# Kernel optimization log

Measured on AMD Instinct MI355X. Metric: run time of the kernel, lower is better.

Reference implementation:

```python
import jax, jax.numpy as jnp
import numpy as np

B, S, H = 2, 2048, 1024
N, DK = 16, 64          # heads, key/value dim (N*DK == H)
DF = 4096               # FFN hidden
SCALE = 1.0 / float(DK) ** 0.5
EPS = 1e-5


def _layer_norm(x, g, b):
    mu = jnp.mean(x, axis=-1, keepdims=True)
    var = jnp.var(x, axis=-1, keepdims=True)
    return (x - mu) * jax.lax.rsqrt(var + EPS) * g + b


def setup_inputs() -> dict:
    key = jax.random.key(0)
    ks = jax.random.split(key, 12)
    s = 0.02
    return {
        "x": jax.random.normal(ks[0], (B, S, H), dtype=jnp.float32),
        "Wq": jax.random.normal(ks[1], (N * DK, H), dtype=jnp.float32) * s,
        "bq": jnp.zeros((N * DK,), jnp.float32),
        "Wk": jax.random.normal(ks[2], (N * DK, H), dtype=jnp.float32) * s,
        "bk": jnp.zeros((N * DK,), jnp.float32),
        "Wv": jax.random.normal(ks[3], (N * DK, H), dtype=jnp.float32) * s,
        "bv": jnp.zeros((N * DK,), jnp.float32),
        "Wo": jax.random.normal(ks[4], (H, N * DK), dtype=jnp.float32) * s,
        "bo": jnp.zeros((H,), jnp.float32),
        "W1": jax.random.normal(ks[5], (DF, H), dtype=jnp.float32) * s,
        "b1": jnp.zeros((DF,), jnp.float32),
        "W2": jax.random.normal(ks[6], (H, DF), dtype=jnp.float32) * s,
        "b2": jnp.zeros((H,), jnp.float32),
        "ln1_g": jnp.ones((H,), jnp.float32),
        "ln1_b": jnp.zeros((H,), jnp.float32),
        "ln2_g": jnp.ones((H,), jnp.float32),
        "ln2_b": jnp.zeros((H,), jnp.float32),
    }


def _mha(x, Wq, bq, Wk, bk, Wv, bv, Wo, bo):
    b = x.shape[0]
    q = (x @ Wq.T + bq).reshape(b, -1, N, DK)  # [B,T,N,DK]
    k = (x @ Wk.T + bk).reshape(b, -1, N, DK)
    v = (x @ Wv.T + bv).reshape(b, -1, N, DK)
    # naive full-score attention, faithful to torch einsum layout
    scores = jnp.einsum('btnd,bsnd->tsbn', q, k) * SCALE  # [T,S,B,N]
    p = jax.nn.softmax(scores, axis=1)                    # softmax over S (dim=1)
    attn = jnp.einsum('tsbn,bsnd->btnd', p, v)            # [B,T,N,DK]
    attn = attn.reshape(b, attn.shape[1], -1)             # [B,T,N*DK]
    return attn @ Wo.T + bo


def reference(x, Wq, bq, Wk, bk, Wv, bv, Wo, bo, W1, b1, W2, b2,
              ln1_g, ln1_b, ln2_g, ln2_b):
    # post-LN encoder layer: x = LN(x + MHA(x)); x = LN(x + FFN(x))
    h = _layer_norm(x + _mha(x, Wq, bq, Wk, bk, Wv, bv, Wo, bo), ln1_g, ln1_b)
    ff = jax.nn.relu(h @ W1.T + b1) @ W2.T + b2
    return _layer_norm(h + ff, ln2_g, ln2_b)
```

## Files before the change

kernel.cpp:

```cpp
#include <hip/hip_runtime.h>
#include <stdint.h>


typedef unsigned short u16;
typedef __bf16 bf16x8 __attribute__((ext_vector_type(8)));
typedef float  f32x4  __attribute__((ext_vector_type(4)));

__device__ __forceinline__ u16 f2bf(float f) {
    unsigned int u = __float_as_uint(f);
    u += 0x7FFFu + ((u >> 16) & 1u);
    return (u16)(u >> 16);
}

__device__ __forceinline__ float bf2f(u16 v) {
    return __uint_as_float((unsigned)v << 16);
}

__device__ __forceinline__ unsigned pack_bf16_hi(float lo, float hi) {
#if __has_builtin(__builtin_amdgcn_perm)
    return __builtin_amdgcn_perm(__float_as_uint(hi), __float_as_uint(lo), 0x07060302u);
#else
    return (__float_as_uint(lo) >> 16) | (__float_as_uint(hi) & 0xFFFF0000u);
#endif
}

__device__ __forceinline__ void async_load16(const u16* g, u16* l) {
    __builtin_amdgcn_global_load_lds(
        (__attribute__((address_space(1))) void*)g,
        (__attribute__((address_space(3))) void*)l, 16, 0, 0);
}

struct CvtArgs {
    const float* src[7];
    u16*         dst[7];
    int          n[7];
};

__global__ __launch_bounds__(256) void k_cvt_all(CvtArgs a) {
    const int seg = blockIdx.y;
    const int i = (blockIdx.x * 256 + threadIdx.x) * 8;
    if (i >= a.n[seg]) return;
    const float* in = a.src[seg];
    u16* out = a.dst[seg];
    float4 x = *(const float4*)(in + i);
    float4 y = *(const float4*)(in + i + 4);
    uint4 o;
    o.x = (unsigned)f2bf(x.x) | ((unsigned)f2bf(x.y) << 16);
    o.y = (unsigned)f2bf(x.z) | ((unsigned)f2bf(x.w) << 16);
    o.z = (unsigned)f2bf(y.x) | ((unsigned)f2bf(y.y) << 16);
    o.w = (unsigned)f2bf(y.z) | ((unsigned)f2bf(y.w) << 16);
    *(uint4*)(out + i) = o;
}

__global__ __launch_bounds__(256) void k_concat3(const float* __restrict__ a,
                                                 const float* __restrict__ b,
                                                 const float* __restrict__ c,
                                                 float* __restrict__ out) {
    int i = blockIdx.x * 256 + threadIdx.x;
    if (i >= 3072) return;
    out[i] = (i < 1024) ? a[i] : (i < 2048 ? b[i - 1024] : c[i - 2048]);
}

template<int OUT_BF16, int RELU>
__global__ __launch_bounds__(256, 4) void k_gemm_bt(
    const u16* __restrict__ A, const u16* __restrict__ Bw,
    const float* __restrict__ bias, void* __restrict__ Y,
    int M, int N, int K)
{
    __shared__ u16 As[128 * 64];
    __shared__ u16 Bs[128 * 64];
    const int tid  = threadIdx.x;
    const int wave = tid >> 6, lane = tid & 63;
    const int lm = lane & 15, lq = lane >> 4;
    const int m0 = blockIdx.x * 128, n0 = blockIdx.y * 128;
    const int wr = (wave >> 1) * 64, wc = (wave & 1) * 64;

    const int ksz = K / gridDim.z;
    const int ks  = blockIdx.z * ksz, ke = ks + ksz;

    const int sr8 = wave * 8 + (lane >> 3);
    const int scx = ((lane & 7) * 8) ^ (((sr8 >> 2) & 3) << 4);
    const size_t arow = (size_t)(m0 + sr8) * K + scx;
    const size_t brow = (size_t)(n0 + sr8) * K + scx;
    const int sw = ((lm >> 2) & 3) << 4;

    f32x4 acc[4][4];
#pragma unroll
    for (int i = 0; i < 4; i++)
#pragma unroll
        for (int j = 0; j < 4; j++) acc[i][j] = (f32x4){0.f, 0.f, 0.f, 0.f};

    for (int k0 = ks; k0 < ke; k0 += 64) {
        __syncthreads();
#pragma unroll
        for (int j = 0; j < 4; j++) {
            async_load16(A  + arow + (size_t)(j * 32) * K + k0, As + j * 2048 + wave * 512);
            async_load16(Bw + brow + (size_t)(j * 32) * K + k0, Bs + j * 2048 + wave * 512);
        }
        __syncthreads();

#pragma unroll
        for (int h = 0; h < 2; h++) {
            const int cofs = (h * 32 + lq * 8) ^ sw;
            bf16x8 af[4], bf[4];
#pragma unroll
            for (int i = 0; i < 4; i++)
                af[i] = *(const bf16x8*)(As + (wr + i * 16 + lm) * 64 + cofs);
#pragma unroll
            for (int j = 0; j < 4; j++)
                bf[j] = *(const bf16x8*)(Bs + (wc + j * 16 + lm) * 64 + cofs);
#pragma unroll
            for (int i = 0; i < 4; i++)
#pragma unroll
                for (int j = 0; j < 4; j++)
                    acc[i][j] = __builtin_amdgcn_mfma_f32_16x16x32_bf16(af[i], bf[j], acc[i][j], 0, 0, 0);
        }
    }

    const float bsc = (blockIdx.z == 0) ? 1.f : 0.f;
    const size_t zoff = (size_t)blockIdx.z * M * N;
#pragma unroll
    for (int i = 0; i < 4; i++) {
        const int mg = m0 + wr + i * 16 + lq * 4;
#pragma unroll
        for (int j = 0; j < 4; j++) {
            const int ng = n0 + wc + j * 16 + lm;
            const float bv = bias[ng] * bsc;
#pragma unroll
            for (int r = 0; r < 4; r++) {
                float v = acc[i][j][r] + bv;
                if (RELU) v = fmaxf(v, 0.f);
                if (OUT_BF16) ((u16*)Y)[zoff + (size_t)(mg + r) * N + ng] = f2bf(v);
                else          ((float*)Y)[zoff + (size_t)(mg + r) * N + ng] = v;
            }
        }
    }
}

__global__ __launch_bounds__(256) void k_transpose_v(const u16* __restrict__ qkv,
                                                     u16* __restrict__ vt) {
    __shared__ u16 T[64 * 72];
    const int tid = threadIdx.x;
    const int t0 = blockIdx.x * 64;
    const int bn = blockIdx.y;
    const int b = bn >> 4, n = bn & 15;
    {
        const int r = tid >> 2, c = (tid & 3) * 16;
        const u16* src = qkv + (size_t)(b * 2048 + t0 + r) * 3072 + 2048 + n * 64 + c;
        *(uint4*)&T[r * 72 + c]     = *(const uint4*)(src);
        *(uint4*)&T[r * 72 + c + 8] = *(const uint4*)(src + 8);
    }
    __syncthreads();
    {
        const int d = tid >> 2, c = (tid & 3) * 16;
        union { u16 h[16]; uint4 v[2]; } tmp;
#pragma unroll
        for (int j = 0; j < 16; j++) {
            const int w = c + j;
            const int k = ((w & 3) << 4) + (w >> 2);
            tmp.h[j] = T[k * 72 + d];
        }
        u16* dst = vt + (size_t)(bn * 64 + d) * 2048 + t0 + c;
        *(uint4*)(dst)     = tmp.v[0];
        *(uint4*)(dst + 8) = tmp.v[1];
    }
}

__global__ __launch_bounds__(256, 2) void k_flash(const u16* __restrict__ qkv,
                                                  const u16* __restrict__ vt,
                                                  u16* __restrict__ attn) {
    __shared__ u16 Ks[2][64 * 72];
    __shared__ u16 Vs[2][64 * 72];
    __shared__ u16 Ps[4 * 32 * 72];
    const int tid = threadIdx.x, wave = tid >> 6, lane = tid & 63;
    const int lm = lane & 15, lq = lane >> 4;
    const int b = blockIdx.z, n = blockIdx.y, qt0 = blockIdx.x * 128;

    bf16x8 qf[2][2];
#pragma unroll
    for (int mh = 0; mh < 2; mh++) {
        const u16* qp = qkv + (size_t)(b * 2048 + qt0 + wave * 32 + mh * 16 + lm) * 3072
                        + n * 64 + lq * 8;
        const bf16x8 q0r = *(const bf16x8*)(qp);
        const bf16x8 q1r = *(const bf16x8*)(qp + 32);
#pragma unroll
        for (int j = 0; j < 8; j++) {
            qf[mh][0][j] = (__bf16)((float)q0r[j] * 0.18033688f);
            qf[mh][1][j] = (__bf16)((float)q1r[j] * 0.18033688f);
        }
    }

    float lsum[2][4];
    f32x4 oacc[2][4];
#pragma unroll
    for (int mh = 0; mh < 2; mh++)
#pragma unroll
        for (int r = 0; r < 4; r++) { lsum[mh][r] = 0.f; }
#pragma unroll
    for (int mh = 0; mh < 2; mh++)
#pragma unroll
        for (int dt = 0; dt < 4; dt++) oacc[mh][dt] = (f32x4){0.f, 0.f, 0.f, 0.f};

    const int sr = tid >> 2, sc = (tid & 3) * 16;
    const u16* kg = qkv + (size_t)(b * 2048 + sr) * 3072 + 1024 + n * 64 + sc;
    const u16* vg = vt + (size_t)((b * 16 + n) * 64 + sr) * 2048 + sc;
    u16* PsW = Ps + wave * 32 * 72;

    {
        uint4 a0 = *(const uint4*)(kg);
        uint4 a1 = *(const uint4*)(kg + 8);
        uint4 b0 = *(const uint4*)(vg);
        uint4 b1 = *(const uint4*)(vg + 8);
        *(uint4*)&Ks[0][sr * 72 + sc]     = a0;
        *(uint4*)&Ks[0][sr * 72 + sc + 8] = a1;
        *(uint4*)&Vs[0][sr * 72 + sc]     = b0;
        *(uint4*)&Vs[0][sr * 72 + sc + 8] = b1;
    }
    uint4 kr0 = *(const uint4*)(kg + 3072);
    uint4 kr1 = *(const uint4*)(kg + 3072 + 8);
    uint4 vr0 = *(const uint4*)(vg + 64);
    uint4 vr1 = *(const uint4*)(vg + 64 + 8);
    __syncthreads();

    int c = 0;
    for (int kt = 0; kt < 2048; kt += 64) {
        if (kt + 64 < 2048) {
            u16* Kd = Ks[c ^ 1];
            u16* Vd = Vs[c ^ 1];
            *(uint4*)&Kd[sr * 72 + sc]     = kr0;
            *(uint4*)&Kd[sr * 72 + sc + 8] = kr1;
            *(uint4*)&Vd[sr * 72 + sc]     = vr0;
            *(uint4*)&Vd[sr * 72 + sc + 8] = vr1;
            if (kt + 128 < 2048) {
                kr0 = *(const uint4*)(kg + (size_t)(kt + 128) * 3072);
                kr1 = *(const uint4*)(kg + (size_t)(kt + 128) * 3072 + 8);
                vr0 = *(const uint4*)(vg + kt + 128);
                vr1 = *(const uint4*)(vg + kt + 128 + 8);
            }
        }

        const u16* Kc = Ks[c];
        const u16* Vc = Vs[c];

        f32x4 sf[2][4];
        __builtin_amdgcn_s_setprio(1);
#pragma unroll
        for (int nt = 0; nt < 4; nt++) {
            const bf16x8 kf0 = *(const bf16x8*)(Kc + (nt * 16 + lm) * 72 + lq * 8);
            const bf16x8 kf1 = *(const bf16x8*)(Kc + (nt * 16 + lm) * 72 + lq * 8 + 32);
#pragma unroll
            for (int mh = 0; mh < 2; mh++) {
                f32x4 z = (f32x4){0.f, 0.f, 0.f, 0.f};
                z = __builtin_amdgcn_mfma_f32_16x16x32_bf16(qf[mh][0], kf0, z, 0, 0, 0);
                z = __builtin_amdgcn_mfma_f32_16x16x32_bf16(qf[mh][1], kf1, z, 0, 0, 0);
                sf[mh][nt] = z;
            }
        }
        __builtin_amdgcn_s_setprio(0);

#pragma unroll
        for (int mh = 0; mh < 2; mh++)
#pragma unroll
            for (int r = 0; r < 4; r++) {
                const float p0 = __builtin_amdgcn_exp2f(sf[mh][0][r]);
                const float p1 = __builtin_amdgcn_exp2f(sf[mh][1][r]);
                const float p2 = __builtin_amdgcn_exp2f(sf[mh][2][r]);
                const float p3 = __builtin_amdgcn_exp2f(sf[mh][3][r]);
                lsum[mh][r] += (p0 + p1) + (p2 + p3);
                uint2 w;
                w.x = pack_bf16_hi(p0, p1);
                w.y = pack_bf16_hi(p2, p3);
                *(uint2*)&PsW[(mh * 16 + lq * 4 + r) * 72 + lm * 4] = w;
            }

        __builtin_amdgcn_s_setprio(1);
#pragma unroll
        for (int s2 = 0; s2 < 2; s2++) {
            bf16x8 pf[2];
#pragma unroll
            for (int mh = 0; mh < 2; mh++)
                pf[mh] = *(const bf16x8*)(PsW + (mh * 16 + lm) * 72 + s2 * 32 + lq * 8);
#pragma unroll
            for (int dt = 0; dt < 4; dt++) {
                const bf16x8 vf = *(const bf16x8*)(Vc + (dt * 16 + lm) * 72 + s2 * 32 + lq * 8);
#pragma unroll
                for (int mh = 0; mh < 2; mh++)
                    oacc[mh][dt] = __builtin_amdgcn_mfma_f32_16x16x32_bf16(pf[mh], vf, oacc[mh][dt], 0, 0, 0);
            }
        }
        __builtin_amdgcn_s_setprio(0);

        __syncthreads();
        c ^= 1;
    }

#pragma unroll
    for (int mh = 0; mh < 2; mh++)
#pragma unroll
        for (int r = 0; r < 4; r++) {
#pragma unroll
            for (int off = 8; off >= 1; off >>= 1)
                lsum[mh][r] += __shfl_xor(lsum[mh][r], off, 16);
            lsum[mh][r] = 1.f / lsum[mh][r];
        }
#pragma unroll
    for (int mh = 0; mh < 2; mh++)
#pragma unroll
        for (int dt = 0; dt < 4; dt++)
#pragma unroll
            for (int r = 0; r < 4; r++) {
                const float o = oacc[mh][dt][r] * lsum[mh][r];
                attn[(size_t)(b * 2048 + qt0 + wave * 32 + mh * 16 + lq * 4 + r) * 1024
                     + n * 64 + dt * 16 + lm] = f2bf(o);
            }
}

template<int WRITE_BF16>
__global__ __launch_bounds__(256) void k_ln_p4(const float* __restrict__ a,
                                               const u16* __restrict__ pb,
                                               const float* __restrict__ g,
                                               const float* __restrict__ be,
                                               float* __restrict__ outf,
                                               u16* __restrict__ outb) {
    const int row = blockIdx.x, tid = threadIdx.x;
    const size_t base = (size_t)row * 1024 + tid * 4;
    const float4 av = *(const float4*)(a + base);
    float x0 = av.x, x1 = av.y, x2 = av.z, x3 = av.w;
#pragma unroll
    for (int z = 0; z < 4; z++) {
        const uint2 w = *(const uint2*)(pb + (size_t)z * 4096 * 1024 + base);
        x0 += __uint_as_float(w.x << 16);
        x1 += __uint_as_float(w.x & 0xFFFF0000u);
        x2 += __uint_as_float(w.y << 16);
        x3 += __uint_as_float(w.y & 0xFFFF0000u);
    }
    float s1 = x0 + x1 + x2 + x3;
    float s2 = x0 * x0 + x1 * x1 + x2 * x2 + x3 * x3;
#pragma unroll
    for (int off = 32; off >= 1; off >>= 1) {
        s1 += __shfl_down(s1, off);
        s2 += __shfl_down(s2, off);
    }
    __shared__ float red[8];
    __shared__ float stats[2];
    const int wave = tid >> 6, lane = tid & 63;
    if (lane == 0) { red[wave] = s1; red[4 + wave] = s2; }
    __syncthreads();
    if (tid == 0) {
        const float t1 = red[0] + red[1] + red[2] + red[3];
        const float t2 = red[4] + red[5] + red[6] + red[7];
        const float mean = t1 * (1.f / 1024.f);
        const float var = t2 * (1.f / 1024.f) - mean * mean;
        stats[0] = mean;
        stats[1] = rsqrtf(var + 1e-5f);
    }
    __syncthreads();
    const float mean = stats[0], rstd = stats[1];
    const int c = tid * 4;
    const float4 gv = *(const float4*)(g + c);
    const float4 bev = *(const float4*)(be + c);
    float4 y;
    y.x = (x0 - mean) * rstd * gv.x + bev.x;
    y.y = (x1 - mean) * rstd * gv.y + bev.y;
    y.z = (x2 - mean) * rstd * gv.z + bev.z;
    y.w = (x3 - mean) * rstd * gv.w + bev.w;
    *(float4*)(outf + base) = y;
    if (WRITE_BF16) {
        uint2 o;
        o.x = (unsigned)f2bf(y.x) | ((unsigned)f2bf(y.y) << 16);
        o.y = (unsigned)f2bf(y.z) | ((unsigned)f2bf(y.w) << 16);
        *(uint2*)(outb + base) = o;
    }
}

extern "C" void kernel_launch(void* const* d_in, const int* in_sizes, int n_in,
                              void* d_out, int out_size, void* d_ws, size_t ws_size,
                              hipStream_t stream) {
    const float* x   = (const float*)d_in[0];
    const float* Wq  = (const float*)d_in[1];
    const float* bq  = (const float*)d_in[2];
    const float* Wk  = (const float*)d_in[3];
    const float* bk  = (const float*)d_in[4];
    const float* Wv  = (const float*)d_in[5];
    const float* bv  = (const float*)d_in[6];
    const float* Wo  = (const float*)d_in[7];
    const float* bo  = (const float*)d_in[8];
    const float* W1  = (const float*)d_in[9];
    const float* b1  = (const float*)d_in[10];
    const float* W2  = (const float*)d_in[11];
    const float* b2  = (const float*)d_in[12];
    const float* g1  = (const float*)d_in[13];
    const float* be1 = (const float*)d_in[14];
    const float* g2  = (const float*)d_in[15];
    const float* be2 = (const float*)d_in[16];

    char* ws = (char*)d_ws;
    const size_t MB = 1024 * 1024;
    u16*   wqkv = (u16*)(ws + 0);
    u16*   wo_b = (u16*)(ws + 6 * MB);
    u16*   w1_b = (u16*)(ws + 8 * MB);
    u16*   w2_b = (u16*)(ws + 16 * MB);
    float* bqkv = (float*)(ws + 24 * MB);
    u16*   xb   = (u16*)(ws + 25 * MB);
    u16*   qkv  = (u16*)(ws + 33 * MB);
    u16*   vt   = (u16*)(ws + 57 * MB);
    u16*   attn = (u16*)(ws + 65 * MB);
    u16*   op4  = (u16*)(ws + 33 * MB);
    float* h    = (float*)(ws + 65 * MB);
    u16*   hb   = (u16*)(ws + 81 * MB);
    u16*   ff1  = (u16*)(ws + 33 * MB);
    u16*   fp4  = (u16*)(ws + 81 * MB);

    CvtArgs ca;
    ca.src[0] = x;  ca.dst[0] = xb;                  ca.n[0] = 4096 * 1024;
    ca.src[1] = Wq; ca.dst[1] = wqkv;                ca.n[1] = 1024 * 1024;
    ca.src[2] = Wk; ca.dst[2] = wqkv + 1024 * 1024;  ca.n[2] = 1024 * 1024;
    ca.src[3] = Wv; ca.dst[3] = wqkv + 2 * 1024 * 1024; ca.n[3] = 1024 * 1024;
    ca.src[4] = Wo; ca.dst[4] = wo_b;                ca.n[4] = 1024 * 1024;
    ca.src[5] = W1; ca.dst[5] = w1_b;                ca.n[5] = 4096 * 1024;
    ca.src[6] = W2; ca.dst[6] = w2_b;                ca.n[6] = 4096 * 1024;
    k_cvt_all<<<dim3(2048, 7), 256, 0, stream>>>(ca);
    k_concat3<<<12, 256, 0, stream>>>(bq, bk, bv, bqkv);

    k_gemm_bt<1, 0><<<dim3(32, 24), 256, 0, stream>>>(
        xb, wqkv, bqkv, qkv, 4096, 3072, 1024);

    k_transpose_v<<<dim3(32, 32), 256, 0, stream>>>(qkv, vt);

    k_flash<<<dim3(16, 16, 2), 256, 0, stream>>>(qkv, vt, attn);

    k_gemm_bt<1, 0><<<dim3(32, 8, 4), 256, 0, stream>>>(
        attn, wo_b, bo, op4, 4096, 1024, 1024);

    k_ln_p4<1><<<4096, 256, 0, stream>>>(x, op4, g1, be1, h, hb);

    k_gemm_bt<1, 1><<<dim3(32, 32), 256, 0, stream>>>(
        hb, w1_b, b1, ff1, 4096, 4096, 1024);

    k_gemm_bt<1, 0><<<dim3(32, 8, 4), 256, 0, stream>>>(
        ff1, w2_b, b2, fp4, 4096, 1024, 4096);

    k_ln_p4<0><<<4096, 256, 0, stream>>>(h, fp4, g2, be2, (float*)d_out, nullptr);
}
```

Measured before the change: 339.0 us.

## Add 256x256 double-buffered async-load GEMM kernel for QKV and FFN projections

```diff
diff --git a/kernel.cpp b/kernel.cpp
--- a/kernel.cpp
+++ b/kernel.cpp
@@ -59,6 +59,145 @@
     int i = blockIdx.x * 256 + threadIdx.x;
     if (i >= 3072) return;
     out[i] = (i < 1024) ? a[i] : (i < 2048 ? b[i - 1024] : c[i - 2048]);
+}
+
+template<int OUT_BF16, int RELU>
+__global__ __launch_bounds__(512, 2) void k_gemm256(
+    const u16* __restrict__ A, const u16* __restrict__ Bw,
+    const float* __restrict__ bias, void* __restrict__ Y,
+    int M, int N, int K)
+{
+    __shared__ u16 As[2][256 * 64];
+    __shared__ u16 Bs[2][256 * 64];
+    const int tid  = threadIdx.x;
+    const int wave = tid >> 6, lane = tid & 63;
+    const int lm = lane & 15, lq = lane >> 4;
+    const int wr = wave >> 2;
+    const int wc = wave & 3;
+    const int m0 = blockIdx.x * 256, n0 = blockIdx.y * 256;
+    const int ksz = K / gridDim.z;
+    const int ks  = blockIdx.z * ksz;
+    const int NT  = ksz >> 6;
+
+    size_t goffA[4], goffB[4];
+#pragma unroll
+    for (int i = 0; i < 4; i++) {
+        const int c = i * 512 + tid;
+        const int row = c >> 3, kcp = c & 7;
+        const int kcl = kcp ^ (row & 7);
+        goffA[i] = (size_t)(m0 + row) * K + kcl * 8;
+        goffB[i] = (size_t)(n0 + row) * K + kcl * 8;
+    }
+
+    const int ach0 = ((0 + lq) ^ (lm & 7)) * 8;
+    const int ach1 = ((4 + lq) ^ (lm & 7)) * 8;
+    const int albase = (wr * 128 + lm) * 64;
+    const int blbase = (wc * 64 + lm) * 64;
+
+    f32x4 acc[8][4];
+#pragma unroll
+    for (int i = 0; i < 8; i++)
+#pragma unroll
+        for (int j = 0; j < 4; j++) acc[i][j] = (f32x4){0.f, 0.f, 0.f, 0.f};
+
+#define STAGE256(T, p)                                                          \
+    {                                                                           \
+        const int k0_ = ks + (T) * 64;                                          \
+        _Pragma("unroll")                                                       \
+        for (int i_ = 0; i_ < 4; i_++) {                                        \
+            async_load16(A  + goffA[i_] + k0_,                                  \
+                         &As[p][(i_ * 512 + wave * 64) * 8]);                   \
+            async_load16(Bw + goffB[i_] + k0_,                                  \
+                         &Bs[p][(i_ * 512 + wave * 64) * 8]);                   \
+        }                                                                       \
+    }
+
+#define LOADQ(dst, q)                                                           \
+    {                                                                           \
+        _Pragma("unroll")                                                       \
+        for (int ii_ = 0; ii_ < 2; ii_++) {                                     \
+            dst[ii_][0] = *(const bf16x8*)(Ab + albase + ((q)*2 + ii_) * 1024 + ach0); \
+            dst[ii_][1] = *(const bf16x8*)(Ab + albase + ((q)*2 + ii_) * 1024 + ach1); \
+        }                                                                       \
+    }
+
+#define MFMAQ(src, q)                                                           \
+    {                                                                           \
+        _Pragma("unroll")                                                       \
+        for (int ii_ = 0; ii_ < 2; ii_++)                                       \
+            _Pragma("unroll")                                                   \
+            for (int j_ = 0; j_ < 4; j_++) {                                    \
+                acc[(q)*2 + ii_][j_] = __builtin_amdgcn_mfma_f32_16x16x32_bf16( \
+                    src[ii_][0], bfr[0][j_], acc[(q)*2 + ii_][j_], 0, 0, 0);    \
+                acc[(q)*2 + ii_][j_] = __builtin_amdgcn_mfma_f32_16x16x32_bf16( \
+                    src[ii_][1], bfr[1][j_], acc[(q)*2 + ii_][j_], 0, 0, 0);    \
+            }                                                                   \
+    }
+
+    STAGE256(0, 0);
+    STAGE256(1, 1);
+    asm volatile("s_waitcnt vmcnt(8)" ::: "memory");
+    __builtin_amdgcn_s_barrier();
+    __builtin_amdgcn_sched_barrier(0);
+
+    for (int T = 0; T < NT; ++T) {
+        const int p = T & 1;
+        const u16* Ab = As[p];
+        const u16* Bb = Bs[p];
+
+        bf16x8 bfr[2][4];
+#pragma unroll
+        for (int j = 0; j < 4; j++) {
+            bfr[0][j] = *(const bf16x8*)(Bb + blbase + j * 1024 + ach0);
+            bfr[1][j] = *(const bf16x8*)(Bb + blbase + j * 1024 + ach1);
+        }
+        bf16x8 aA[2][2], aB[2][2];
+        LOADQ(aA, 0);
+        LOADQ(aB, 1);
+        MFMAQ(aA, 0);
+        LOADQ(aA, 2);
+        MFMAQ(aB, 1);
+        LOADQ(aB, 3);
+        MFMAQ(aA, 2);
+        MFMAQ(aB, 3);
+
+        __builtin_amdgcn_sched_barrier(0);
+        __builtin_amdgcn_s_barrier();
+        __builtin_amdgcn_sched_barrier(0);
+
+        if (T + 2 < NT) {
+            STAGE256(T + 2, p);
+            asm volatile("s_waitcnt vmcnt(8)" ::: "memory");
+            __builtin_amdgcn_s_barrier();
+            __builtin_amdgcn_sched_barrier(0);
+        } else if (T + 1 < NT) {
+            asm volatile("s_waitcnt vmcnt(0)" ::: "memory");
+            __builtin_amdgcn_s_barrier();
+            __builtin_amdgcn_sched_barrier(0);
+        }
+    }
+#undef STAGE256
+#undef LOADQ
+#undef MFMAQ
+
+    const float bsc = (blockIdx.z == 0) ? 1.f : 0.f;
+    const size_t zoff = (size_t)blockIdx.z * M * N;
+#pragma unroll
+    for (int i = 0; i < 8; i++) {
+        const int mg = m0 + wr * 128 + i * 16 + lq * 4;
+#pragma unroll
+        for (int j = 0; j < 4; j++) {
+            const int ng = n0 + wc * 64 + j * 16 + lm;
+            const float bv = bias[ng] * bsc;
+#pragma unroll
+            for (int r = 0; r < 4; r++) {
+                float v = acc[i][j][r] + bv;
+                if (RELU) v = fmaxf(v, 0.f);
+                if (OUT_BF16) ((u16*)Y)[zoff + (size_t)(mg + r) * N + ng] = f2bf(v);
+                else          ((float*)Y)[zoff + (size_t)(mg + r) * N + ng] = v;
+            }
+        }
+    }
 }
 
 template<int OUT_BF16, int RELU>
@@ -422,7 +561,7 @@
     k_cvt_all<<<dim3(2048, 7), 256, 0, stream>>>(ca);
     k_concat3<<<12, 256, 0, stream>>>(bq, bk, bv, bqkv);
 
-    k_gemm_bt<1, 0><<<dim3(32, 24), 256, 0, stream>>>(
+    k_gemm256<1, 0><<<dim3(16, 12), 512, 0, stream>>>(
         xb, wqkv, bqkv, qkv, 4096, 3072, 1024);
 
     k_transpose_v<<<dim3(32, 32), 256, 0, stream>>>(qkv, vt);
@@ -434,10 +573,10 @@
 
     k_ln_p4<1><<<4096, 256, 0, stream>>>(x, op4, g1, be1, h, hb);
 
-    k_gemm_bt<1, 1><<<dim3(32, 32), 256, 0, stream>>>(
+    k_gemm256<1, 1><<<dim3(16, 16), 512, 0, stream>>>(
         hb, w1_b, b1, ff1, 4096, 4096, 1024);
 
-    k_gemm_bt<1, 0><<<dim3(32, 8, 4), 256, 0, stream>>>(
+    k_gemm256<1, 0><<<dim3(16, 4, 4), 512, 0, stream>>>(
         ff1, w2_b, b2, fp4, 4096, 1024, 4096);
 
     k_ln_p4<0><<<4096, 256, 0, stream>>>(h, fp4, g2, be2, (float*)d_out, nullptr);
```

After: 332.0 us. 2.1% less time.

## Split flash attention over key halves with larger query tiles and a combine pass

Applied to the files above, without the earlier changes.

```diff
diff --git a/kernel.cpp b/kernel.cpp
--- a/kernel.cpp
+++ b/kernel.cpp
@@ -168,18 +168,21 @@
 
 __global__ __launch_bounds__(256, 2) void k_flash(const u16* __restrict__ qkv,
                                                   const u16* __restrict__ vt,
-                                                  u16* __restrict__ attn) {
+                                                  float* __restrict__ opart,
+                                                  float* __restrict__ lsb) {
     __shared__ u16 Ks[2][64 * 72];
     __shared__ u16 Vs[2][64 * 72];
-    __shared__ u16 Ps[4 * 32 * 72];
+    __shared__ u16 Ps[4 * 64 * 72];
     const int tid = threadIdx.x, wave = tid >> 6, lane = tid & 63;
     const int lm = lane & 15, lq = lane >> 4;
-    const int b = blockIdx.z, n = blockIdx.y, qt0 = blockIdx.x * 128;
-
-    bf16x8 qf[2][2];
-#pragma unroll
-    for (int mh = 0; mh < 2; mh++) {
-        const u16* qp = qkv + (size_t)(b * 2048 + qt0 + wave * 32 + mh * 16 + lm) * 3072
+    const int zz = blockIdx.z;
+    const int b = zz >> 1, kvh = zz & 1;
+    const int n = blockIdx.y, qt0 = blockIdx.x * 256;
+
+    bf16x8 qf[4][2];
+#pragma unroll
+    for (int mh = 0; mh < 4; mh++) {
+        const u16* qp = qkv + (size_t)(b * 2048 + qt0 + wave * 64 + mh * 16 + lm) * 3072
                         + n * 64 + lq * 8;
         const bf16x8 q0r = *(const bf16x8*)(qp);
         const bf16x8 q1r = *(const bf16x8*)(qp + 32);
@@ -190,21 +193,21 @@
         }
     }
 
-    float lsum[2][4];
-    f32x4 oacc[2][4];
-#pragma unroll
-    for (int mh = 0; mh < 2; mh++)
-#pragma unroll
-        for (int r = 0; r < 4; r++) { lsum[mh][r] = 0.f; }
-#pragma unroll
-    for (int mh = 0; mh < 2; mh++)
+    float lsum[4][4];
+    f32x4 oacc[4][4];
+#pragma unroll
+    for (int mh = 0; mh < 4; mh++)
+#pragma unroll
+        for (int r = 0; r < 4; r++) lsum[mh][r] = 0.f;
+#pragma unroll
+    for (int mh = 0; mh < 4; mh++)
 #pragma unroll
         for (int dt = 0; dt < 4; dt++) oacc[mh][dt] = (f32x4){0.f, 0.f, 0.f, 0.f};
 
     const int sr = tid >> 2, sc = (tid & 3) * 16;
-    const u16* kg = qkv + (size_t)(b * 2048 + sr) * 3072 + 1024 + n * 64 + sc;
-    const u16* vg = vt + (size_t)((b * 16 + n) * 64 + sr) * 2048 + sc;
-    u16* PsW = Ps + wave * 32 * 72;
+    const u16* kg = qkv + (size_t)(b * 2048 + kvh * 1024 + sr) * 3072 + 1024 + n * 64 + sc;
+    const u16* vg = vt + (size_t)((b * 16 + n) * 64 + sr) * 2048 + kvh * 1024 + sc;
+    u16* PsW = Ps + wave * 64 * 72;
 
     {
         uint4 a0 = *(const uint4*)(kg);
@@ -223,15 +226,15 @@
     __syncthreads();
 
     int c = 0;
-    for (int kt = 0; kt < 2048; kt += 64) {
-        if (kt + 64 < 2048) {
+    for (int kt = 0; kt < 1024; kt += 64) {
+        if (kt + 64 < 1024) {
             u16* Kd = Ks[c ^ 1];
             u16* Vd = Vs[c ^ 1];
             *(uint4*)&Kd[sr * 72 + sc]     = kr0;
             *(uint4*)&Kd[sr * 72 + sc + 8] = kr1;
             *(uint4*)&Vd[sr * 72 + sc]     = vr0;
             *(uint4*)&Vd[sr * 72 + sc + 8] = vr1;
-            if (kt + 128 < 2048) {
+            if (kt + 128 < 1024) {
                 kr0 = *(const uint4*)(kg + (size_t)(kt + 128) * 3072);
                 kr1 = *(const uint4*)(kg + (size_t)(kt + 128) * 3072 + 8);
                 vr0 = *(const uint4*)(vg + kt + 128);
@@ -242,49 +245,51 @@
         const u16* Kc = Ks[c];
         const u16* Vc = Vs[c];
 
-        f32x4 sf[2][4];
-        __builtin_amdgcn_s_setprio(1);
+        bf16x8 kf0[4], kf1[4];
 #pragma unroll
         for (int nt = 0; nt < 4; nt++) {
-            const bf16x8 kf0 = *(const bf16x8*)(Kc + (nt * 16 + lm) * 72 + lq * 8);
-            const bf16x8 kf1 = *(const bf16x8*)(Kc + (nt * 16 + lm) * 72 + lq * 8 + 32);
-#pragma unroll
-            for (int mh = 0; mh < 2; mh++) {
+            kf0[nt] = *(const bf16x8*)(Kc + (nt * 16 + lm) * 72 + lq * 8);
+            kf1[nt] = *(const bf16x8*)(Kc + (nt * 16 + lm) * 72 + lq * 8 + 32);
+        }
+
+#pragma unroll
+        for (int mh = 0; mh < 4; mh++) {
+            f32x4 s[4];
+            __builtin_amdgcn_s_setprio(1);
+#pragma unroll
+            for (int nt = 0; nt < 4; nt++) {
                 f32x4 z = (f32x4){0.f, 0.f, 0.f, 0.f};
-                z = __builtin_amdgcn_mfma_f32_16x16x32_bf16(qf[mh][0], kf0, z, 0, 0, 0);
-                z = __builtin_amdgcn_mfma_f32_16x16x32_bf16(qf[mh][1], kf1, z, 0, 0, 0);
-                sf[mh][nt] = z;
-            }
-        }
-        __builtin_amdgcn_s_setprio(0);
-
-#pragma unroll
-        for (int mh = 0; mh < 2; mh++)
+                z = __builtin_amdgcn_mfma_f32_16x16x32_bf16(qf[mh][0], kf0[nt], z, 0, 0, 0);
+                z = __builtin_amdgcn_mfma_f32_16x16x32_bf16(qf[mh][1], kf1[nt], z, 0, 0, 0);
+                s[nt] = z;
+            }
+            __builtin_amdgcn_s_setprio(0);
 #pragma unroll
             for (int r = 0; r < 4; r++) {
-                const float p0 = __builtin_amdgcn_exp2f(sf[mh][0][r]);
-                const float p1 = __builtin_amdgcn_exp2f(sf[mh][1][r]);
-                const float p2 = __builtin_amdgcn_exp2f(sf[mh][2][r]);
-                const float p3 = __builtin_amdgcn_exp2f(sf[mh][3][r]);
+                const float p0 = __builtin_amdgcn_exp2f(s[0][r]);
+                const float p1 = __builtin_amdgcn_exp2f(s[1][r]);
+                const float p2 = __builtin_amdgcn_exp2f(s[2][r]);
+                const float p3 = __builtin_amdgcn_exp2f(s[3][r]);
                 lsum[mh][r] += (p0 + p1) + (p2 + p3);
                 uint2 w;
                 w.x = pack_bf16_hi(p0, p1);
                 w.y = pack_bf16_hi(p2, p3);
                 *(uint2*)&PsW[(mh * 16 + lq * 4 + r) * 72 + lm * 4] = w;
             }
+        }
 
         __builtin_amdgcn_s_setprio(1);
 #pragma unroll
         for (int s2 = 0; s2 < 2; s2++) {
-            bf16x8 pf[2];
-#pragma unroll
-            for (int mh = 0; mh < 2; mh++)
+            bf16x8 pf[4];
+#pragma unroll
+            for (int mh = 0; mh < 4; mh++)
                 pf[mh] = *(const bf16x8*)(PsW + (mh * 16 + lm) * 72 + s2 * 32 + lq * 8);
 #pragma unroll
             for (int dt = 0; dt < 4; dt++) {
                 const bf16x8 vf = *(const bf16x8*)(Vc + (dt * 16 + lm) * 72 + s2 * 32 + lq * 8);
 #pragma unroll
-                for (int mh = 0; mh < 2; mh++)
+                for (int mh = 0; mh < 4; mh++)
                     oacc[mh][dt] = __builtin_amdgcn_mfma_f32_16x16x32_bf16(pf[mh], vf, oacc[mh][dt], 0, 0, 0);
             }
         }
@@ -295,24 +300,48 @@
     }
 
 #pragma unroll
-    for (int mh = 0; mh < 2; mh++)
+    for (int mh = 0; mh < 4; mh++)
 #pragma unroll
         for (int r = 0; r < 4; r++) {
 #pragma unroll
             for (int off = 8; off >= 1; off >>= 1)
                 lsum[mh][r] += __shfl_xor(lsum[mh][r], off, 16);
-            lsum[mh][r] = 1.f / lsum[mh][r];
-        }
-#pragma unroll
-    for (int mh = 0; mh < 2; mh++)
+        }
+
+    const size_t half = (size_t)kvh * 4096 * 1024;
+#pragma unroll
+    for (int mh = 0; mh < 4; mh++)
 #pragma unroll
         for (int dt = 0; dt < 4; dt++)
 #pragma unroll
             for (int r = 0; r < 4; r++) {
-                const float o = oacc[mh][dt][r] * lsum[mh][r];
-                attn[(size_t)(b * 2048 + qt0 + wave * 32 + mh * 16 + lq * 4 + r) * 1024
-                     + n * 64 + dt * 16 + lm] = f2bf(o);
-            }
+                opart[half + (size_t)(b * 2048 + qt0 + wave * 64 + mh * 16 + lq * 4 + r) * 1024
+                      + n * 64 + dt * 16 + lm] = oacc[mh][dt][r];
+            }
+    if (lm == 0) {
+#pragma unroll
+        for (int mh = 0; mh < 4; mh++)
+#pragma unroll
+            for (int r = 0; r < 4; r++) {
+                const int qrow = qt0 + wave * 64 + mh * 16 + lq * 4 + r;
+                lsb[(size_t)kvh * 4096 * 16 + (size_t)(b * 2048 + qrow) * 16 + n] = lsum[mh][r];
+            }
+    }
+}
+
+__global__ __launch_bounds__(256) void k_att_combine(const float* __restrict__ opart,
+                                                     const float* __restrict__ lsb,
+                                                     u16* __restrict__ attn) {
+    const int row = blockIdx.x, tid = threadIdx.x;
+    const int n = tid >> 4, d0 = (tid & 15) * 4;
+    const size_t o = (size_t)row * 1024 + n * 64 + d0;
+    const float4 a = *(const float4*)(opart + o);
+    const float4 c = *(const float4*)(opart + (size_t)4096 * 1024 + o);
+    const float inv = 1.f / (lsb[(size_t)row * 16 + n] + lsb[(size_t)4096 * 16 + row * 16 + n]);
+    uint2 w;
+    w.x = (unsigned)f2bf((a.x + c.x) * inv) | ((unsigned)f2bf((a.y + c.y) * inv) << 16);
+    w.y = (unsigned)f2bf((a.z + c.z) * inv) | ((unsigned)f2bf((a.w + c.w) * inv) << 16);
+    *(uint2*)(attn + o) = w;
 }
 
 template<int WRITE_BF16>
@@ -396,20 +425,22 @@
 
     char* ws = (char*)d_ws;
     const size_t MB = 1024 * 1024;
-    u16*   wqkv = (u16*)(ws + 0);
-    u16*   wo_b = (u16*)(ws + 6 * MB);
-    u16*   w1_b = (u16*)(ws + 8 * MB);
-    u16*   w2_b = (u16*)(ws + 16 * MB);
-    float* bqkv = (float*)(ws + 24 * MB);
-    u16*   xb   = (u16*)(ws + 25 * MB);
-    u16*   qkv  = (u16*)(ws + 33 * MB);
-    u16*   vt   = (u16*)(ws + 57 * MB);
-    u16*   attn = (u16*)(ws + 65 * MB);
-    u16*   op4  = (u16*)(ws + 33 * MB);
-    float* h    = (float*)(ws + 65 * MB);
-    u16*   hb   = (u16*)(ws + 81 * MB);
-    u16*   ff1  = (u16*)(ws + 33 * MB);
-    u16*   fp4  = (u16*)(ws + 81 * MB);
+    u16*   wqkv  = (u16*)(ws + 0);
+    u16*   wo_b  = (u16*)(ws + 6 * MB);
+    u16*   w1_b  = (u16*)(ws + 8 * MB);
+    u16*   w2_b  = (u16*)(ws + 16 * MB);
+    float* bqkv  = (float*)(ws + 24 * MB);
+    float* lsb   = (float*)(ws + 24 * MB + 512 * 1024);
+    u16*   xb    = (u16*)(ws + 25 * MB);
+    u16*   qkv   = (u16*)(ws + 33 * MB);
+    u16*   vt    = (u16*)(ws + 57 * MB);
+    float* opart = (float*)(ws + 65 * MB);
+    u16*   attn  = (u16*)(ws + 97 * MB);
+    u16*   op4   = (u16*)(ws + 33 * MB);
+    float* h     = (float*)(ws + 65 * MB);
+    u16*   hb    = (u16*)(ws + 81 * MB);
+    u16*   ff1   = (u16*)(ws + 33 * MB);
+    u16*   fp4   = (u16*)(ws + 81 * MB);
 
     CvtArgs ca;
     ca.src[0] = x;  ca.dst[0] = xb;                  ca.n[0] = 4096 * 1024;
@@ -427,7 +458,9 @@
 
     k_transpose_v<<<dim3(32, 32), 256, 0, stream>>>(qkv, vt);
 
-    k_flash<<<dim3(16, 16, 2), 256, 0, stream>>>(qkv, vt, attn);
+    k_flash<<<dim3(8, 16, 4), 256, 0, stream>>>(qkv, vt, opart, lsb);
+
+    k_att_combine<<<4096, 256, 0, stream>>>(opart, lsb, attn);
 
     k_gemm_bt<1, 0><<<dim3(32, 8, 4), 256, 0, stream>>>(
         attn, wo_b, bo, op4, 4096, 1024, 1024);
```

Measured after the change: 337.8 us. About the same (-0.4%).
